# Optimization experiments

Hardware: AMD Instinct MI355X
Metric: run time of the kernel (lower is better)

## Reference

```python
import jax, jax.numpy as jnp
import numpy as np

R = 16       # voxel resolution
CH = 64      # channels
NSAMPLE = 16
PROJ = 3


def _bn(x, p, eps):
    # p: [4, C] rows = (gamma, beta, running_mean, running_var); eval-mode BN
    g, b, m, v = p
    sh = [1] * x.ndim
    sh[1] = -1
    return (x - m.reshape(sh)) * (g.reshape(sh) * jax.lax.rsqrt(v.reshape(sh) + eps)) + b.reshape(sh)


def _gather_ch(x, flat_idx):
    # x: [B, C, M], flat_idx: [B, L] -> [B, C, L]
    B, C, _ = x.shape
    idx = jnp.broadcast_to(flat_idx[:, None, :], (B, C, flat_idx.shape[1]))
    return jnp.take_along_axis(x, idx, axis=2)


def _pvb_forward(x, xyz, idx, w3d1, b3d1, bn3d1, w3d2, b3d2, bn3d2, proj_w1, proj_bn, proj_w2, pt_bn):
    B, C, N = x.shape
    r = R
    # ---------- voxelization (coords detached, normalize=False) ----------
    nc = xyz - xyz.mean(axis=2, keepdims=True)
    nc = jnp.clip((nc + 1.0) * 0.5 * r, 0.0, r - 1.0)
    nc = jax.lax.stop_gradient(nc)                        # [B,3,N] float in [0, r-1]
    vi = jnp.round(nc).astype(jnp.int32)
    flat = (vi[:, 0] * r + vi[:, 1]) * r + vi[:, 2]       # [B,N]
    seg = (flat + jnp.arange(B, dtype=jnp.int32)[:, None] * (r ** 3)).reshape(-1)
    feats = x.transpose(0, 2, 1).reshape(B * N, C)
    sums = jax.ops.segment_sum(feats, seg, num_segments=B * r ** 3)
    cnts = jax.ops.segment_sum(jnp.ones((B * N,), x.dtype), seg, num_segments=B * r ** 3)
    v = (sums / jnp.maximum(cnts, 1.0)[:, None]).reshape(B, r, r, r, C).transpose(0, 4, 1, 2, 3)
    # ---------- depthwise Conv3d -> BN3d -> LeakyReLU (x2) ----------
    dn = ('NCDHW', 'OIDHW', 'NCDHW')
    v = jax.lax.conv_general_dilated(v, w3d1, (1, 1, 1), 'SAME', dimension_numbers=dn,
                                     feature_group_count=C) + b3d1.reshape(1, C, 1, 1, 1)
    v = jax.nn.leaky_relu(_bn(v, bn3d1, 1e-4), 0.1)
    v = jax.lax.conv_general_dilated(v, w3d2, (1, 1, 1), 'SAME', dimension_numbers=dn,
                                     feature_group_count=C) + b3d2.reshape(1, C, 1, 1, 1)
    v = jax.nn.leaky_relu(_bn(v, bn3d2, 1e-4), 0.1)
    # ---------- trilinear devoxelize ----------
    vf = v.reshape(B, C, r ** 3)
    lo = jnp.floor(nc).astype(jnp.int32)
    fr = nc - lo
    hi = jnp.minimum(lo + 1, r - 1)
    p_v_x = jnp.zeros((B, C, N), x.dtype)
    for dx in (0, 1):
        for dy in (0, 1):
            for dz in (0, 1):
                xi = hi[:, 0] if dx else lo[:, 0]
                yi = hi[:, 1] if dy else lo[:, 1]
                zi = hi[:, 2] if dz else lo[:, 2]
                w = ((fr[:, 0] if dx else 1.0 - fr[:, 0]) *
                     (fr[:, 1] if dy else 1.0 - fr[:, 1]) *
                     (fr[:, 2] if dz else 1.0 - fr[:, 2]))
                p_v_x = p_v_x + w[:, None, :] * _gather_ch(vf, (xi * r + yi) * r + zi)
    # ---------- neighbor gather (precomputed ball-query idx) ----------
    K = idx.shape[-1]
    flat_nb = idx.reshape(B, N * K)
    x_j = _gather_ch(x, flat_nb).reshape(B, C, N, K)
    xyz_j = _gather_ch(xyz, flat_nb).reshape(B, 3, N, K)
    dp1 = xyz_j - xyz[:, :, :, None]                      # [B,3,N,K]
    df = x_j - x[:, :, :, None]                           # [B,C,N,K]
    # proj_conv: 1x1 conv -> BN2d -> ReLU -> 1x1 conv
    h = jnp.einsum('oc,bcnk->bonk', proj_w1, df)
    h = jax.nn.relu(_bn(h, proj_bn, 1e-5))
    dp2 = jnp.einsum('oc,bcnk->bonk', proj_w2, h)         # [B,3,N,K]
    dp = jnp.concatenate([dp1, dp2], axis=1)              # [B,6,N,K]
    # repeat_interleave of the 6 channels up to C (last gets remainder)
    part = 6
    rep = C // part
    repeats = np.array([rep] * (part - 1) + [C - rep * (part - 1)])
    w = jnp.repeat(dp, repeats, axis=1, total_repeat_length=C)
    x_j = x_j * w
    x_j = jax.nn.relu(_bn(x_j, pt_bn, 1e-5))              # proj_transform
    p_p_x = x_j.max(axis=-1)                              # max-pool over neighbors
    return p_v_x + p_p_x                                  # agg_way == 'add'


def setup_inputs() -> dict:
    key = jax.random.key(0)
    ks = jax.random.split(key, 16)
    B, C, N, K = 4, CH, 16384, NSAMPLE

    def bn_params(k, c):
        k1, k2, k3, k4 = jax.random.split(k, 4)
        return jnp.stack([1.0 + 0.1 * jax.random.normal(k1, (c,), jnp.float32),
                          0.1 * jax.random.normal(k2, (c,), jnp.float32),
                          0.1 * jax.random.normal(k3, (c,), jnp.float32),
                          jax.random.uniform(k4, (c,), jnp.float32, 0.5, 1.5)])

    return dict(
        x=jax.random.normal(ks[0], (B, C, N), jnp.float32),
        xyz=jax.random.uniform(ks[1], (B, 3, N), jnp.float32, -1.0, 1.0),
        idx=jax.random.randint(ks[2], (B, N, K), 0, N, jnp.int32),
        w3d1=0.1 * jax.random.normal(ks[3], (C, 1, 3, 3, 3), jnp.float32),
        b3d1=0.01 * jax.random.normal(ks[4], (C,), jnp.float32),
        bn3d1=bn_params(ks[5], C),
        w3d2=0.1 * jax.random.normal(ks[6], (C, 1, 3, 3, 3), jnp.float32),
        b3d2=0.01 * jax.random.normal(ks[7], (C,), jnp.float32),
        bn3d2=bn_params(ks[8], C),
        proj_w1=0.1 * jax.random.normal(ks[9], (PROJ, C), jnp.float32),
        proj_bn=bn_params(ks[10], PROJ),
        proj_w2=0.3 * jax.random.normal(ks[11], (PROJ, PROJ), jnp.float32),
        pt_bn=bn_params(ks[12], C),
    )


def reference(x, xyz, idx, w3d1, b3d1, bn3d1, w3d2, b3d2, bn3d2, proj_w1, proj_bn, proj_w2, pt_bn):
    return _pvb_forward(x, xyz, idx, w3d1, b3d1, bn3d1, w3d2, b3d2, bn3d2, proj_w1, proj_bn, proj_w2, pt_bn)
```

## Files before the change

kernel.cpp:

```cpp
#include <hip/hip_runtime.h>

namespace {
constexpr int B_  = 4;
constexpr int C_  = 64;
constexpr int N_  = 16384;
constexpr int K_  = 16;
constexpr int R3_ = 4096;

constexpr int OFF_MEANS = 0;
constexpr int OFF_XT    = 16;
constexpr int OFF_PTS   = OFF_XT   + B_*N_*C_/2;
constexpr int OFF_PTSH  = OFF_PTS  + B_*N_*8;
constexpr int OFF_DVT   = OFF_PTSH + B_*N_*4;
constexpr int OFF_SUMS  = OFF_DVT  + B_*N_*8;
constexpr int OFF_CNTS  = OFF_SUMS + B_*R3_*C_;
constexpr int OFF_VT16  = OFF_CNTS + B_*R3_;
constexpr int FILL_FLOATS = B_*R3_*C_ + B_*R3_;
constexpr int FILL_BLOCKS = FILL_FLOATS / (256 * 4);
}

__device__ __forceinline__ unsigned short f2bf(float f) {
  unsigned u = __float_as_uint(f);
  return (unsigned short)((u + 0x7FFFu + ((u >> 16) & 1u)) >> 16);
}
__device__ __forceinline__ float bf2f(unsigned short h) {
  return __uint_as_float(((unsigned)h) << 16);
}
__device__ __forceinline__ unsigned cvtpk_bf16(float lo, float hi) {
  unsigned r;
  asm("v_cvt_pk_bf16_f32 %0, %1, %2" : "=v"(r) : "v"(lo), "v"(hi));
  return r;
}
__device__ __forceinline__ float bflo(unsigned u) { return __uint_as_float(u << 16); }
__device__ __forceinline__ float bfhi(unsigned u) { return __uint_as_float(u & 0xffff0000u); }

__global__ __launch_bounds__(256) void k_init(
    const float* __restrict__ xyz, float* __restrict__ means,
    float* __restrict__ fill) {
  const int blk = blockIdx.x;
  if (blk >= 12) {
    const int base = (blk - 12) * (256 * 4) + threadIdx.x * 4;
    *(float4*)(fill + base) = make_float4(0.f, 0.f, 0.f, 0.f);
    return;
  }
  __shared__ double red[256];
  const float* p = xyz + blk * N_;
  double s = 0.0;
  for (int i = threadIdx.x; i < N_; i += 256) s += (double)p[i];
  red[threadIdx.x] = s;
  __syncthreads();
  for (int st = 128; st; st >>= 1) {
    if (threadIdx.x < st) red[threadIdx.x] += red[threadIdx.x + st];
    __syncthreads();
  }
  if (threadIdx.x == 0) means[blk] = (float)(red[0] * (1.0 / (double)N_));
}

__global__ __launch_bounds__(256) void k_prep(
    const float* __restrict__ x, const float* __restrict__ xyz,
    const float* __restrict__ pw1, const float* __restrict__ means,
    unsigned short* __restrict__ xT, float* __restrict__ pts,
    unsigned* __restrict__ ptsh, unsigned* __restrict__ dvt,
    float* __restrict__ sums, float* __restrict__ cnts) {
  __shared__ float tile[64 * 65];
  __shared__ float ncs[3][64];
  __shared__ float xys[3][64];
  __shared__ float hps[3][64];
  __shared__ int   flats[64];

  const int t   = threadIdx.x;
  const int blk = blockIdx.x;
  const int b   = blk >> 8;
  const int n0  = (blk & 255) << 6;

#pragma unroll
  for (int i = 0; i < 4; ++i) {
    int c = i * 16 + (t >> 4);
    int j4 = (t & 15) * 4;
    float4 v = *(const float4*)&x[((size_t)(b * C_ + c)) * N_ + n0 + j4];
    tile[c * 65 + j4 + 0] = v.x;
    tile[c * 65 + j4 + 1] = v.y;
    tile[c * 65 + j4 + 2] = v.z;
    tile[c * 65 + j4 + 3] = v.w;
  }
  __syncthreads();

  unsigned* __restrict__ xT32 = (unsigned*)xT;
#pragma unroll
  for (int i = 0; i < 8; ++i) {
    int p = i * 8 + (t >> 5);
    int c2 = (t & 31) * 2;
    unsigned pk = cvtpk_bf16(tile[c2 * 65 + p], tile[(c2 + 1) * 65 + p]);
    xT32[((size_t)(b * N_ + n0 + p)) * 32 + (t & 31)] = pk;
  }

  if (t < 192) {
    int p = t & 63, q = t >> 6;
    float s = 0.f;
#pragma unroll
    for (int c = 0; c < 64; ++c) s = fmaf(pw1[q * 64 + c], tile[c * 65 + p], s);
    size_t pb = ((size_t)(b * N_ + n0 + p)) * 8;
    pts[pb + 3 + q] = s;
    hps[q][p] = s;
    float v = xyz[((size_t)(b * 3 + q)) * N_ + n0 + p];
    pts[pb + q] = v;
    xys[q][p] = v;
    float nc = fminf(fmaxf((v - means[b * 3 + q] + 1.0f) * 8.0f, 0.0f), 15.0f);
    ncs[q][p] = nc;
  } else {
    int p = t & 63;
    size_t pb = ((size_t)(b * N_ + n0 + p)) * 8;
    pts[pb + 6] = 0.f;
    pts[pb + 7] = 0.f;
  }
  __syncthreads();

  if (t < 64) {
    const float nc0 = ncs[0][t], nc1 = ncs[1][t], nc2 = ncs[2][t];
    int vx = (int)rintf(nc0);
    int vy = (int)rintf(nc1);
    int vz = (int)rintf(nc2);
    int f = (vx * 16 + vy) * 16 + vz;
    flats[t] = f;
    atomicAdd(&cnts[b * R3_ + f], 1.0f);
    uint4 r;
    r.x = cvtpk_bf16(xys[0][t], xys[1][t]);
    r.y = cvtpk_bf16(xys[2][t], hps[0][t]);
    r.z = cvtpk_bf16(hps[1][t], hps[2][t]);
    r.w = 0u;
    *(uint4*)&ptsh[((size_t)(b * N_ + n0 + t)) * 4] = r;
    int lx = (int)nc0, ly = (int)nc1, lz = (int)nc2;
    float fx = nc0 - (float)lx, fy = nc1 - (float)ly, fz = nc2 - (float)lz;
    unsigned base = (unsigned)((lx * 16 + ly) * 16 + lz);
    unsigned w0 = base | (((unsigned)f2bf(fz)) << 16);
    unsigned w1 = cvtpk_bf16(fx, fy);
    *(uint2*)&dvt[((size_t)(b * N_ + n0 + t)) * 2] = make_uint2(w0, w1);
  }
  __syncthreads();

  const int w = t >> 6, lane = t & 63;
#pragma unroll
  for (int i = 0; i < 16; ++i) {
    int p = w * 16 + i;
    int f = flats[p];
    atomicAdd(&sums[((size_t)(b * R3_ + f)) * C_ + lane], tile[lane * 65 + p]);
  }
}

__global__ __launch_bounds__(256) void k_tr(
    const float* __restrict__ sums, const float* __restrict__ cnts,
    unsigned* __restrict__ vT16) {
  __shared__ float tile[64 * 65];
  __shared__ float rs[64];
  const int t = threadIdx.x;
  const int b = blockIdx.x >> 6;
  const int v0 = (blockIdx.x & 63) << 6;

#pragma unroll
  for (int i = 0; i < 16; ++i) {
    int r = i * 4 + (t >> 6);
    int c = t & 63;
    tile[r * 65 + c] = sums[((size_t)(b * R3_ + v0 + r)) * C_ + c];
  }
  if (t < 64) rs[t] = 1.0f / fmaxf(cnts[b * R3_ + v0 + t], 1.0f);
  __syncthreads();

#pragma unroll
  for (int i = 0; i < 8; ++i) {
    int d = t + i * 256;
    int c = d >> 5, vp = (d & 31) * 2;
    unsigned pk = cvtpk_bf16(tile[vp * 65 + c] * rs[vp],
                             tile[(vp + 1) * 65 + c] * rs[vp + 1]);
    vT16[((size_t)(b * C_ + c)) * 2048 + (v0 >> 1) + (d & 31)] = pk;
  }
}

__global__ __launch_bounds__(256, 8) void k_point(
    const unsigned short* __restrict__ xT, const float* __restrict__ pts,
    const unsigned* __restrict__ ptsh, const int* __restrict__ idx,
    const float* __restrict__ pbn, const float* __restrict__ pw2,
    const float* __restrict__ ptbn, float* __restrict__ out) {
  __shared__ unsigned w6[3][513];
  __shared__ int      jarr[512];
  __shared__ float    outT[64 * 33];

  const int t = threadIdx.x;
  const int blk = blockIdx.x;
  const int xcd = blk & 7;
  const int b = xcd >> 1;
  const int t32 = ((blk >> 3) << 1) | (xcd & 1);
  const int n0 = t32 * 32;

  const float psc0 = pbn[0] * rsqrtf(pbn[9]  + 1e-5f);
  const float psc1 = pbn[1] * rsqrtf(pbn[10] + 1e-5f);
  const float psc2 = pbn[2] * rsqrtf(pbn[11] + 1e-5f);
  const float pof0 = pbn[3] - pbn[6] * psc0;
  const float pof1 = pbn[4] - pbn[7] * psc1;
  const float pof2 = pbn[5] - pbn[8] * psc2;
  float W2r[9];
#pragma unroll
  for (int i = 0; i < 9; ++i) W2r[i] = pw2[i];

  const float* __restrict__ ptsb = pts + (size_t)b * N_ * 8;
  const unsigned* __restrict__ ptshb = ptsh + (size_t)b * N_ * 4;

#pragma unroll
  for (int rep = 0; rep < 2; ++rep) {
    const int q = t + rep * 256;
    const int p = q >> 4;
    const int n = n0 + p;
    const int j = idx[(size_t)b * N_ * K_ + (size_t)n0 * K_ + q];
    jarr[q] = j;
    uint4 q4 = *(const uint4*)(ptshb + (size_t)j * 4);
    const float qx0 = bflo(q4.x), qx1 = bfhi(q4.x);
    const float qx2 = bflo(q4.y), qh0 = bfhi(q4.y);
    const float qh1 = bflo(q4.z), qh2 = bfhi(q4.z);
    const float* ir = ptsb + (size_t)n * 8;
    float4 pa = *(const float4*)ir;
    float4 pb = *(const float4*)(ir + 4);
    float d0 = qx0 - pa.x, d1 = qx1 - pa.y, d2 = qx2 - pa.z;
    float c0 = pof0 - psc0 * pa.w;
    float c1 = pof1 - psc1 * pb.x;
    float c2 = pof2 - psc2 * pb.y;
    float h0 = fmaxf(fmaf(qh0, psc0, c0), 0.f);
    float h1 = fmaxf(fmaf(qh1, psc1, c1), 0.f);
    float h2 = fmaxf(fmaf(qh2, psc2, c2), 0.f);
    float e0 = fmaf(W2r[0], h0, fmaf(W2r[1], h1, W2r[2] * h2));
    float e1 = fmaf(W2r[3], h0, fmaf(W2r[4], h1, W2r[5] * h2));
    float e2 = fmaf(W2r[6], h0, fmaf(W2r[7], h1, W2r[8] * h2));
    w6[0][q] = cvtpk_bf16(d0, d1);
    w6[1][q] = cvtpk_bf16(d2, e0);
    w6[2][q] = cvtpk_bf16(e1, e2);
  }
  __syncthreads();

  const int w = t >> 6, lane = t & 63;
  const int widx = lane < 20 ? 0 : lane < 40 ? 1 : 2;
  const bool hi = (lane >= 10 && lane < 20) || (lane >= 30 && lane < 40) || (lane >= 50);
  const unsigned shl = hi ? 0u : 16u;
  const float ts = ptbn[lane] * rsqrtf(ptbn[192 + lane] + 1e-5f);
  const float td = ptbn[64 + lane] - ptbn[128 + lane] * ts;
  const unsigned short* __restrict__ xTb = xT + (size_t)b * N_ * C_;

#pragma unroll
  for (int i = 0; i < 8; ++i) {
    const int p = i * 4 + w;
    const int pq = p * 16;

    unsigned short xjv[16];
#pragma unroll
    for (int k = 0; k < 16; ++k)
      xjv[k] = xTb[(size_t)jarr[pq + k] * C_ + lane];

    float pm = 0.f;
#pragma unroll
    for (int k = 0; k < 16; ++k) {
      float wf = __uint_as_float(w6[widx][pq + k] << shl);
      pm = fmaxf(pm, fmaf(bf2f(xjv[k]) * wf, ts, td));
    }

    outT[lane * 33 + p] = pm;
  }
  __syncthreads();

#pragma unroll
  for (int i = 0; i < 8; ++i) {
    int c = i * 8 + (t >> 5);
    int col = t & 31;
    out[((size_t)(b * C_ + c)) * N_ + n0 + col] = outT[c * 33 + col];
  }
}

__global__ __launch_bounds__(512) void k_convdevox(
    const unsigned* __restrict__ vT16,
    const float* __restrict__ w3d1, const float* __restrict__ b3d1,
    const float* __restrict__ bn1, const float* __restrict__ w3d2,
    const float* __restrict__ b3d2, const float* __restrict__ bn2,
    const unsigned* __restrict__ dvt, float* __restrict__ out) {
  __shared__ float va[18 * 18 * 20];
  __shared__ float vb[18 * 18 * 20];
  __shared__ float vls[4370];
  const int t = threadIdx.x;
  const int b = blockIdx.x >> 6;
  const int c = blockIdx.x & 63;

  float W1[27], W2[27];
#pragma unroll
  for (int i = 0; i < 27; ++i) { W1[i] = w3d1[c * 27 + i]; W2[i] = w3d2[c * 27 + i]; }
  const float s1 = bn1[c] / sqrtf(bn1[192 + c] + 1e-4f);
  const float d1 = (b3d1[c] - bn1[128 + c]) * s1 + bn1[64 + c];
  const float s2 = bn2[c] / sqrtf(bn2[192 + c] + 1e-4f);
  const float d2 = (b3d2[c] - bn2[128 + c]) * s2 + bn2[64 + c];

  for (int i = t; i < 18 * 18 * 20; i += 512) { va[i] = 0.f; vb[i] = 0.f; }
  if (t < 274) vls[4096 + t] = 0.f;
  const unsigned* __restrict__ vrow = vT16 + ((size_t)(b * C_ + c)) * 2048;
  __syncthreads();

#pragma unroll
  for (int i = 0; i < 4; ++i) {
    int d = t + i * 512;
    unsigned u = vrow[d];
    int vox0 = d * 2;
    int z = vox0 & 15, yy = (vox0 >> 4) & 15, xx = vox0 >> 8;
    int base = ((xx + 1) * 18 + (yy + 1)) * 20 + (z + 1);
    va[base]     = bflo(u);
    va[base + 1] = bfhi(u);
  }
  __syncthreads();

  const int x = t >> 5, y = (t >> 1) & 15, z0 = (t & 1) * 8;
  float acc[8];

#pragma unroll
  for (int z = 0; z < 8; ++z) acc[z] = 0.f;
#pragma unroll
  for (int dx = 0; dx < 3; ++dx)
#pragma unroll
    for (int dy = 0; dy < 3; ++dy) {
      const float* row = &va[((x + dx) * 18 + (y + dy)) * 20 + z0];
      float wv[12];
      *(float4*)&wv[0] = *(const float4*)&row[0];
      *(float4*)&wv[4] = *(const float4*)&row[4];
      *(float4*)&wv[8] = *(const float4*)&row[8];
      const float k0 = W1[(dx * 3 + dy) * 3 + 0];
      const float k1 = W1[(dx * 3 + dy) * 3 + 1];
      const float k2 = W1[(dx * 3 + dy) * 3 + 2];
#pragma unroll
      for (int z = 0; z < 8; ++z)
        acc[z] = fmaf(k0, wv[z], fmaf(k1, wv[z + 1], fmaf(k2, wv[z + 2], acc[z])));
    }
  {
    const int wb = ((x + 1) * 18 + (y + 1)) * 20 + 1 + z0;
#pragma unroll
    for (int z = 0; z < 8; ++z) {
      float tt = acc[z] * s1 + d1;
      vb[wb + z] = tt > 0.f ? tt : 0.1f * tt;
    }
  }
  __syncthreads();

#pragma unroll
  for (int z = 0; z < 8; ++z) acc[z] = 0.f;
#pragma unroll
  for (int dx = 0; dx < 3; ++dx)
#pragma unroll
    for (int dy = 0; dy < 3; ++dy) {
      const float* row = &vb[((x + dx) * 18 + (y + dy)) * 20 + z0];
      float wv[12];
      *(float4*)&wv[0] = *(const float4*)&row[0];
      *(float4*)&wv[4] = *(const float4*)&row[4];
      *(float4*)&wv[8] = *(const float4*)&row[8];
      const float k0 = W2[(dx * 3 + dy) * 3 + 0];
      const float k1 = W2[(dx * 3 + dy) * 3 + 1];
      const float k2 = W2[(dx * 3 + dy) * 3 + 2];
#pragma unroll
      for (int z = 0; z < 8; ++z)
        acc[z] = fmaf(k0, wv[z], fmaf(k1, wv[z + 1], fmaf(k2, wv[z + 2], acc[z])));
    }
  {
    const int vbase = (x * 16 + y) * 16 + z0;
#pragma unroll
    for (int z = 0; z < 8; ++z) {
      float tt = acc[z] * s2 + d2;
      vls[vbase + z] = tt > 0.f ? tt : 0.1f * tt;
    }
  }
  __syncthreads();

  const uint2* __restrict__ dv2 = (const uint2*)(dvt + (size_t)b * N_ * 2);
  float* __restrict__ orow = out + ((size_t)(b * C_ + c)) * N_;
#pragma unroll 4
  for (int i = 0; i < 32; ++i) {
    const int n = t + i * 512;
    uint2 r = dv2[n];
    float o = orow[n];
    const int base = (int)(r.x & 0xffffu);
    const float fz = bfhi(r.x);
    const float fx = bflo(r.y), fy = bfhi(r.y);
    const float* v0 = &vls[base];
    float a0 = v0[0],   a1 = v0[1];
    float b0 = v0[16],  b1 = v0[17];
    float c0 = v0[256], c1 = v0[257];
    float d0 = v0[272], d1 = v0[273];
    float zA = fmaf(fz, a1 - a0, a0);
    float zB = fmaf(fz, b1 - b0, b0);
    float zC = fmaf(fz, c1 - c0, c0);
    float zD = fmaf(fz, d1 - d0, d0);
    float yAB = fmaf(fy, zB - zA, zA);
    float yCD = fmaf(fy, zD - zC, zC);
    orow[n] = o + fmaf(fx, yCD - yAB, yAB);
  }
}

extern "C" void kernel_launch(void* const* d_in, const int* in_sizes, int n_in,
                              void* d_out, int out_size, void* d_ws, size_t ws_size,
                              hipStream_t stream) {
  const float* x     = (const float*)d_in[0];
  const float* xyz   = (const float*)d_in[1];
  const int*   idx   = (const int*)  d_in[2];
  const float* w3d1  = (const float*)d_in[3];
  const float* b3d1  = (const float*)d_in[4];
  const float* bn3d1 = (const float*)d_in[5];
  const float* w3d2  = (const float*)d_in[6];
  const float* b3d2  = (const float*)d_in[7];
  const float* bn3d2 = (const float*)d_in[8];
  const float* pw1   = (const float*)d_in[9];
  const float* pbn   = (const float*)d_in[10];
  const float* pw2   = (const float*)d_in[11];
  const float* ptbn  = (const float*)d_in[12];
  float* out = (float*)d_out;
  float* ws  = (float*)d_ws;

  k_init<<<dim3(12 + FILL_BLOCKS), dim3(256), 0, stream>>>(
      xyz, ws + OFF_MEANS, ws + OFF_SUMS);
  k_prep<<<dim3(B_ * N_ / 64), dim3(256), 0, stream>>>(
      x, xyz, pw1, ws + OFF_MEANS, (unsigned short*)(ws + OFF_XT), ws + OFF_PTS,
      (unsigned*)(ws + OFF_PTSH), (unsigned*)(ws + OFF_DVT),
      ws + OFF_SUMS, ws + OFF_CNTS);
  k_tr<<<dim3(B_ * 64), dim3(256), 0, stream>>>(
      ws + OFF_SUMS, ws + OFF_CNTS, (unsigned*)(ws + OFF_VT16));
  k_point<<<dim3(B_ * N_ / 32), dim3(256), 0, stream>>>(
      (const unsigned short*)(ws + OFF_XT), ws + OFF_PTS,
      (const unsigned*)(ws + OFF_PTSH), idx, pbn, pw2, ptbn, out);
  k_convdevox<<<dim3(B_ * C_), dim3(512), 0, stream>>>(
      (const unsigned*)(ws + OFF_VT16), w3d1, b3d1, bn3d1, w3d2, b3d2, bn3d2,
      (const unsigned*)(ws + OFF_DVT), out);
}
```

Baseline: 85.64 us.

## Pre-scale gathered features by BN scale and gather bf16 pairs per lane

Folds the point BN scale into the bf16 transposed features in k_prep, so the per-neighbor max only needs a multiply and the shift and ReLU are applied once after the max. In k_point each lane now loads a 32-bit pair of channels instead of a 16-bit value, and two points are handled per wavefront (half-waves), halving gather instructions. This relies on max commuting with the additive shift, and changes rounding because the scale is applied before bf16 conversion.

New measurement: 82.12 us. -4.1%, faster.

```diff
diff --git a/kernel.cpp b/kernel.cpp
--- a/kernel.cpp
+++ b/kernel.cpp
@@ -59,6 +59,7 @@
 __global__ __launch_bounds__(256) void k_prep(
     const float* __restrict__ x, const float* __restrict__ xyz,
     const float* __restrict__ pw1, const float* __restrict__ means,
+    const float* __restrict__ ptbn,
     unsigned short* __restrict__ xT, float* __restrict__ pts,
     unsigned* __restrict__ ptsh, unsigned* __restrict__ dvt,
     float* __restrict__ sums, float* __restrict__ cnts) {
@@ -66,12 +67,15 @@
   __shared__ float ncs[3][64];
   __shared__ float xys[3][64];
   __shared__ float hps[3][64];
+  __shared__ float tss[64];
   __shared__ int   flats[64];
 
   const int t   = threadIdx.x;
   const int blk = blockIdx.x;
   const int b   = blk >> 8;
   const int n0  = (blk & 255) << 6;
+
+  if (t < 64) tss[t] = ptbn[t] * rsqrtf(ptbn[192 + t] + 1e-5f);
 
 #pragma unroll
   for (int i = 0; i < 4; ++i) {
@@ -90,7 +94,8 @@
   for (int i = 0; i < 8; ++i) {
     int p = i * 8 + (t >> 5);
     int c2 = (t & 31) * 2;
-    unsigned pk = cvtpk_bf16(tile[c2 * 65 + p], tile[(c2 + 1) * 65 + p]);
+    unsigned pk = cvtpk_bf16(tile[c2 * 65 + p] * tss[c2],
+                             tile[(c2 + 1) * 65 + p] * tss[c2 + 1]);
     xT32[((size_t)(b * N_ + n0 + p)) * 32 + (t & 31)] = pk;
   }
 
@@ -235,31 +240,44 @@
   __syncthreads();
 
   const int w = t >> 6, lane = t & 63;
-  const int widx = lane < 20 ? 0 : lane < 40 ? 1 : 2;
-  const bool hi = (lane >= 10 && lane < 20) || (lane >= 30 && lane < 40) || (lane >= 50);
+  const int half = lane >> 5;
+  const int d = lane & 31;
+  const int widx = d < 10 ? 0 : d < 20 ? 1 : 2;
+  const bool hi = (d >= 5 && d < 10) || (d >= 15 && d < 20) || (d >= 25);
   const unsigned shl = hi ? 0u : 16u;
-  const float ts = ptbn[lane] * rsqrtf(ptbn[192 + lane] + 1e-5f);
-  const float td = ptbn[64 + lane] - ptbn[128 + lane] * ts;
-  const unsigned short* __restrict__ xTb = xT + (size_t)b * N_ * C_;
-
-#pragma unroll
-  for (int i = 0; i < 8; ++i) {
-    const int p = i * 4 + w;
+  const int c0i = 2 * d, c1i = 2 * d + 1;
+  const float ts0 = ptbn[c0i] * rsqrtf(ptbn[192 + c0i] + 1e-5f);
+  const float ts1 = ptbn[c1i] * rsqrtf(ptbn[192 + c1i] + 1e-5f);
+  const float td0 = ptbn[64 + c0i] - ptbn[128 + c0i] * ts0;
+  const float td1 = ptbn[64 + c1i] - ptbn[128 + c1i] * ts1;
+  const unsigned* __restrict__ xT32b =
+      (const unsigned*)xT + (size_t)b * N_ * 32;
+
+#pragma unroll
+  for (int i = 0; i < 4; ++i) {
+    const int p = i * 8 + w + half * 4;
     const int pq = p * 16;
 
-    unsigned short xjv[16];
-#pragma unroll
-    for (int k = 0; k < 16; ++k)
-      xjv[k] = xTb[(size_t)jarr[pq + k] * C_ + lane];
-
-    float pm = 0.f;
+    unsigned xju[16], wfu[16];
 #pragma unroll
     for (int k = 0; k < 16; ++k) {
-      float wf = __uint_as_float(w6[widx][pq + k] << shl);
-      pm = fmaxf(pm, fmaf(bf2f(xjv[k]) * wf, ts, td));
-    }
-
-    outT[lane * 33 + p] = pm;
+      const int j = jarr[pq + k];
+      xju[k] = xT32b[(size_t)j * 32 + d];
+      wfu[k] = w6[widx][pq + k];
+    }
+
+    float pm0 = -3.0e38f, pm1 = -3.0e38f;
+#pragma unroll
+    for (int k = 0; k < 16; ++k) {
+      float wf = __uint_as_float(wfu[k] << shl);
+      float x0 = __uint_as_float(xju[k] << 16);
+      float x1 = __uint_as_float(xju[k] & 0xffff0000u);
+      pm0 = fmaxf(pm0, x0 * wf);
+      pm1 = fmaxf(pm1, x1 * wf);
+    }
+
+    outT[c0i * 33 + p] = fmaxf(pm0 + td0, 0.f);
+    outT[c1i * 33 + p] = fmaxf(pm1 + td1, 0.f);
   }
   __syncthreads();
 
@@ -415,7 +433,8 @@
   k_init<<<dim3(12 + FILL_BLOCKS), dim3(256), 0, stream>>>(
       xyz, ws + OFF_MEANS, ws + OFF_SUMS);
   k_prep<<<dim3(B_ * N_ / 64), dim3(256), 0, stream>>>(
-      x, xyz, pw1, ws + OFF_MEANS, (unsigned short*)(ws + OFF_XT), ws + OFF_PTS,
+      x, xyz, pw1, ws + OFF_MEANS, ptbn,
+      (unsigned short*)(ws + OFF_XT), ws + OFF_PTS,
       (unsigned*)(ws + OFF_PTSH), (unsigned*)(ws + OFF_DVT),
       ws + OFF_SUMS, ws + OFF_CNTS);
   k_tr<<<dim3(B_ * 64), dim3(256), 0, stream>>>(
```
